# Optimization experiments

Hardware: AMD Instinct MI355X
Metric: run time of the kernel (lower is better)

Reference implementation:

```python
import jax, jax.numpy as jnp
import numpy as np


def setup_inputs() -> dict:
    key = jax.random.key(0)
    k1, k2, k3 = jax.random.split(key, 3)
    B, T, C = 4, 2048, 1024
    dim = C
    x = jax.random.normal(k1, (B, T, C), dtype=jnp.float32)
    # torch nn.Linear weight layout: [out_features, in_features], scaled like kaiming-uniform-ish
    w_qkv = jax.random.normal(k2, (3 * dim, dim), dtype=jnp.float32) * (1.0 / np.sqrt(dim))
    w_out = jax.random.normal(k3, (dim, dim), dtype=jnp.float32) * (1.0 / np.sqrt(dim))
    return {"x": x, "w_qkv": w_qkv, "w_out": w_out}


def reference(x, w_qkv, w_out):
    B, T, C = x.shape
    n_heads = 16
    head_dim = C // n_heads

    qkv = jnp.einsum("btc,dc->btd", x, w_qkv)  # [B,T,3C]
    q, k, v = jnp.split(qkv, 3, axis=-1)

    def split_heads(t):
        return t.reshape(B, T, n_heads, head_dim).transpose(0, 2, 1, 3)  # [B,H,T,hd]

    q, k, v = split_heads(q), split_heads(k), split_heads(v)

    scale = 1.0 / np.sqrt(head_dim).astype(np.float32)
    scores = jnp.einsum("bhqd,bhkd->bhqk", q, k) * scale  # [B,H,T,T]
    causal = jnp.tril(jnp.ones((T, T), dtype=bool))
    scores = jnp.where(causal, scores, jnp.finfo(scores.dtype).min)
    attn = jax.nn.softmax(scores, axis=-1)
    out = jnp.einsum("bhqk,bhkd->bhqd", attn, v)  # [B,H,T,hd]
    out = out.transpose(0, 2, 1, 3).reshape(B, T, C)
    return jnp.einsum("btc,dc->btd", out, w_out)
```

## Files before the change

kernel.cpp:

```cpp
#include <hip/hip_runtime.h>
#include <hip/hip_bf16.h>


typedef __attribute__((ext_vector_type(8))) short bf16x8;
typedef __attribute__((ext_vector_type(4))) float f32x4;
typedef __attribute__((ext_vector_type(16))) float f32x16;
typedef __attribute__((ext_vector_type(2))) unsigned uint2v;

#define GLOBAL_AS __attribute__((address_space(1)))
#define LDS_AS __attribute__((address_space(3)))

__device__ __forceinline__ unsigned short f2b_rne(float f) {
  unsigned u = __float_as_uint(f);
  unsigned r = u + 0x7fffu + ((u >> 16) & 1u);
  return (unsigned short)(r >> 16);
}

__device__ __forceinline__ unsigned cvt_pk_bf16(float lo, float hi) {
  unsigned r;
  asm("v_cvt_pk_bf16_f32 %0, %1, %2" : "=v"(r) : "v"(lo), "v"(hi));
  return r;
}

__device__ __forceinline__ void gload_lds16(const void* g, void* l) {
  __builtin_amdgcn_global_load_lds((const GLOBAL_AS void*)g, (LDS_AS void*)l, 16, 0, 0);
}

__global__ void f32_to_bf16_vec(const float* __restrict__ src,
                                unsigned short* __restrict__ dst, int n4) {
  int i = blockIdx.x * blockDim.x + threadIdx.x;
  int stride = gridDim.x * blockDim.x;
  for (; i < n4; i += stride) {
    float4 v = reinterpret_cast<const float4*>(src)[i];
    ushort4 o;
    o.x = f2b_rne(v.x); o.y = f2b_rne(v.y);
    o.z = f2b_rne(v.z); o.w = f2b_rne(v.w);
    reinterpret_cast<ushort4*>(dst)[i] = o;
  }
}

__global__ __launch_bounds__(256)
void v_transpose(const unsigned short* __restrict__ qkv,
                 unsigned short* __restrict__ vt) {
  __shared__ __align__(16) unsigned short Ts[64][64];
  const int tc = blockIdx.x, bh = blockIdx.y;
  const int b = bh >> 4, hed = bh & 15;
  const int t0 = tc * 64;
  const int tid = threadIdx.x;
  {
    const int r = tid >> 2, cb = (tid & 3) * 2;
    const unsigned short* src =
        qkv + (size_t)(b * 2048 + t0 + r) * 3072 + 2048 + hed * 64;
    bf16x8 v0 = *(const bf16x8*)(src + cb * 8);
    bf16x8 v1 = *(const bf16x8*)(src + cb * 8 + 8);
    *(bf16x8*)&Ts[r][(cb ^ (r & 7)) * 8] = v0;
    *(bf16x8*)&Ts[r][((cb + 1) ^ (r & 7)) * 8] = v1;
  }
  __syncthreads();
  const int d = tid >> 2;
  unsigned short* dst = vt + ((size_t)bh * 64 + d) * 2048 + t0;
#pragma unroll
  for (int tb2 = 0; tb2 < 2; ++tb2) {
    int tb = (tid & 3) * 2 + tb2;
    union { unsigned short s[8]; bf16x8 v; } o;
#pragma unroll
    for (int i = 0; i < 8; ++i) {
      int row = tb * 8 + i;
      o.s[i] = Ts[row][(((d >> 3) ^ (row & 7)) * 8) + (d & 7)];
    }
    *(bf16x8*)(dst + tb * 8) = o.v;
  }
}

template <int OUT_BF16>
__global__ __launch_bounds__(256)
void gemm_nt(const unsigned short* __restrict__ A,
             const unsigned short* __restrict__ B,
             void* __restrict__ Cout, int M, int N, int K) {
  __shared__ __align__(16) unsigned short As[128][32];
  __shared__ __align__(16) unsigned short Bs[128][32];
  const int tid = threadIdx.x;
  const int w = tid >> 6, lane = tid & 63;
  const int l16 = lane & 15, lg = lane >> 4;
  const int wrow = (w >> 1) * 64, wcol = (w & 1) * 64;
  const int m0 = blockIdx.y * 128, n0 = blockIdx.x * 128;

  f32x4 acc[4][4] = {};

  auto stage = [&](int k0) {
#pragma unroll
    for (int c2 = 0; c2 < 2; ++c2) {
      int c = 2 * w + c2;
      const unsigned short* ga =
          A + (size_t)(m0 + 16 * c + (lane >> 2)) * K + k0 + (lane & 3) * 8;
      gload_lds16(ga, &As[16 * c][0]);
      const unsigned short* gb =
          B + (size_t)(n0 + 16 * c + (lane >> 2)) * K + k0 + (lane & 3) * 8;
      gload_lds16(gb, &Bs[16 * c][0]);
    }
  };

  stage(0);
  __syncthreads();
  const int nk = K >> 5;
  for (int ks = 0; ks < nk; ++ks) {
    bf16x8 af[4], bfr[4];
#pragma unroll
    for (int mi = 0; mi < 4; ++mi)
      af[mi] = *(const bf16x8*)&As[wrow + mi * 16 + l16][lg * 8];
#pragma unroll
    for (int ni = 0; ni < 4; ++ni)
      bfr[ni] = *(const bf16x8*)&Bs[wcol + ni * 16 + l16][lg * 8];
    __syncthreads();
    if (ks + 1 < nk) stage((ks + 1) * 32);
#pragma unroll
    for (int mi = 0; mi < 4; ++mi)
#pragma unroll
      for (int ni = 0; ni < 4; ++ni)
        acc[mi][ni] = __builtin_amdgcn_mfma_f32_16x16x32_bf16(
            af[mi], bfr[ni], acc[mi][ni], 0, 0, 0);
    __syncthreads();
  }

#pragma unroll
  for (int mi = 0; mi < 4; ++mi) {
#pragma unroll
    for (int ni = 0; ni < 4; ++ni) {
#pragma unroll
      for (int j = 0; j < 4; ++j) {
        int row = m0 + wrow + mi * 16 + lg * 4 + j;
        int col = n0 + wcol + ni * 16 + l16;
        if (OUT_BF16) {
          ((unsigned short*)Cout)[(size_t)row * N + col] =
              f2b_rne(acc[mi][ni][j]);
        } else {
          ((float*)Cout)[(size_t)row * N + col] = acc[mi][ni][j];
        }
      }
    }
  }
}

__global__ __launch_bounds__(256)
void attn_fwd(const unsigned short* __restrict__ qkv,
              const unsigned short* __restrict__ vt,
              unsigned short* __restrict__ out) {
  const int T = 2048, C3 = 3072;
  __shared__ __align__(16) unsigned short Ks[2][64][64];
  __shared__ __align__(16) unsigned short Vs[2][64][64];
  __shared__ float Bc[4][32];

  const int tid = threadIdx.x, w = tid >> 6, lane = tid & 63;
  const int l31 = lane & 31, h = lane >> 5;
  const int wgid = (blockIdx.x & 7) * 128 + (blockIdx.x >> 3);
  const int qt = 15 - (wgid & 15);
  const int bh = wgid >> 4;
  const int b = bh >> 4, hed = bh & 15;
  const int qw = qt * 128 + w * 32;
  const size_t rowbase = (size_t)b * T * C3;
  const int hoff = hed * 64;
  const unsigned short* vbase = vt + (size_t)bh * 64 * 2048;
  const float c2 = 0.18033688f;

  auto stageK = [&](int kv0, int buf) {
#pragma unroll
    for (int pp = 0; pp < 2; ++pp) {
      int chunk = w * 2 + pp;
      int row = chunk * 8 + (lane >> 3);
      int blk = (lane & 7) ^ (lane >> 3);
      gload_lds16(
          qkv + rowbase + (size_t)(kv0 + row) * C3 + 1024 + hoff + blk * 8,
          &Ks[buf][chunk * 8][0]);
    }
  };
  auto stageV = [&](int kv0, int buf) {
#pragma unroll
    for (int pp = 0; pp < 2; ++pp) {
      int chunk = w * 2 + pp;
      int drow = chunk * 8 + (lane >> 3);
      int blk = (lane & 7) ^ (lane >> 3);
      gload_lds16(vbase + (size_t)drow * 2048 + kv0 + blk * 8,
                  &Vs[buf][chunk * 8][0]);
    }
  };

  bf16x8 qf[4];
  {
    const unsigned short* qp =
        qkv + rowbase + (size_t)(qw + l31) * C3 + hoff + h * 8;
#pragma unroll
    for (int s = 0; s < 4; ++s) qf[s] = *(const bf16x8*)(qp + 16 * s);
  }

  f32x16 oacc[2] = {};
  float m_r = -1e30f, sum = 0.f;

  stageK(0, 0);
  stageV(0, 0);

  int cur = 0;
  const int ntiles = qt * 2 + 2;
  for (int t = 0; t < ntiles; ++t) {
    const int kv0 = t * 64;
    __builtin_amdgcn_s_barrier();
    if (t + 1 < ntiles) {
      stageK(kv0 + 64, cur ^ 1);
      stageV(kv0 + 64, cur ^ 1);
      asm volatile("s_waitcnt vmcnt(4)" ::: "memory");
    } else {
      asm volatile("s_waitcnt vmcnt(0)" ::: "memory");
    }
    __builtin_amdgcn_s_barrier();
    __builtin_amdgcn_sched_barrier(0);

    if (kv0 <= qw) {
      f32x16 sacc[2] = {};
      __builtin_amdgcn_s_setprio(1);
#pragma unroll
      for (int s = 0; s < 4; ++s) {
#pragma unroll
        for (int kt = 0; kt < 2; ++kt) {
          int row = kt * 32 + l31;
          int blk = (2 * s + h) ^ (row & 7);
          bf16x8 kf = *(const bf16x8*)&Ks[cur][row][blk * 8];
          sacc[kt] = __builtin_amdgcn_mfma_f32_32x32x16_bf16(kf, qf[s],
                                                             sacc[kt], 0, 0, 0);
        }
      }
      __builtin_amdgcn_s_setprio(0);
      if (kv0 + 64 > qw) {
        int q_abs = qw + l31;
#pragma unroll
        for (int kt = 0; kt < 2; ++kt)
#pragma unroll
          for (int r = 0; r < 16; ++r) {
            int kv_abs = kv0 + kt * 32 + (r & 3) + 8 * (r >> 2) + 4 * h;
            if (kv_abs > q_abs) sacc[kt][r] = -1e30f;
          }
      }
      float mx[8];
#pragma unroll
      for (int g = 0; g < 8; ++g)
        mx[g] = fmaxf(fmaxf(sacc[g >> 2][(g & 3) * 4 + 0],
                            sacc[g >> 2][(g & 3) * 4 + 1]),
                      fmaxf(sacc[g >> 2][(g & 3) * 4 + 2],
                            sacc[g >> 2][(g & 3) * 4 + 3]));
      float tm = fmaxf(fmaxf(fmaxf(mx[0], mx[1]), fmaxf(mx[2], mx[3])),
                       fmaxf(fmaxf(mx[4], mx[5]), fmaxf(mx[6], mx[7])));
      tm = fmaxf(tm, __shfl_xor(tm, 32));
      if (t == 0) {
        m_r = tm;
      } else if (!__all(tm <= m_r + 16.0f)) {
        float mnew = fmaxf(m_r, tm);
        float corr = __builtin_amdgcn_exp2f((m_r - mnew) * c2);
        sum *= corr;
        if (h == 0) Bc[w][l31] = corr;
        m_r = mnew;
        asm volatile("s_waitcnt lgkmcnt(0)" ::: "memory");
#pragma unroll
        for (int r = 0; r < 16; ++r) {
          float cr = Bc[w][(r & 3) + 8 * (r >> 2) + 4 * h];
          oacc[0][r] *= cr;
          oacc[1][r] *= cr;
        }
      }
      float m2 = m_r * c2;
      float s0 = 0.f, s1 = 0.f, s2 = 0.f, s3 = 0.f;
#pragma unroll
      for (int kt = 0; kt < 2; ++kt)
#pragma unroll
        for (int r = 0; r < 16; r += 4) {
          float p0 = __builtin_amdgcn_exp2f(fmaf(sacc[kt][r + 0], c2, -m2));
          float p1 = __builtin_amdgcn_exp2f(fmaf(sacc[kt][r + 1], c2, -m2));
          float p2 = __builtin_amdgcn_exp2f(fmaf(sacc[kt][r + 2], c2, -m2));
          float p3 = __builtin_amdgcn_exp2f(fmaf(sacc[kt][r + 3], c2, -m2));
          sacc[kt][r + 0] = p0; sacc[kt][r + 1] = p1;
          sacc[kt][r + 2] = p2; sacc[kt][r + 3] = p3;
          s0 += p0; s1 += p1; s2 += p2; s3 += p3;
        }
      float sl = (s0 + s1) + (s2 + s3);
      sum += sl + __shfl_xor(sl, 32);
      unsigned pk[16];
#pragma unroll
      for (int kt = 0; kt < 2; ++kt)
#pragma unroll
        for (int r = 0; r < 16; r += 2)
          pk[kt * 8 + (r >> 1)] = cvt_pk_bf16(sacc[kt][r], sacc[kt][r + 1]);
      __builtin_amdgcn_s_setprio(1);
#pragma unroll
      for (int sg = 0; sg < 4; ++sg) {
        const int kt = sg >> 1, s = sg & 1;
        const int base = kt * 8 + 4 * s;
        uint2v r02 = __builtin_amdgcn_permlane32_swap(pk[base], pk[base + 2],
                                                      false, false);
        uint2v r13 = __builtin_amdgcn_permlane32_swap(pk[base + 1], pk[base + 3],
                                                      false, false);
        union { unsigned u[4]; bf16x8 v; } A;
        A.u[0] = r02.x; A.u[1] = r13.x;
        A.u[2] = r02.y; A.u[3] = r13.y;
#pragma unroll
        for (int dt = 0; dt < 2; ++dt) {
          int d = dt * 32 + l31;
          int blk = (2 * sg + h) ^ (d & 7);
          bf16x8 vf = *(const bf16x8*)&Vs[cur][d][blk * 8];
          oacc[dt] = __builtin_amdgcn_mfma_f32_32x32x16_bf16(A.v, vf,
                                                             oacc[dt], 0, 0, 0);
        }
      }
      __builtin_amdgcn_s_setprio(0);
    }
    cur ^= 1;
  }

  if (h == 0) Bc[w][l31] = 1.0f / sum;
  asm volatile("s_waitcnt lgkmcnt(0)" ::: "memory");
#pragma unroll
  for (int r = 0; r < 16; ++r) {
    int ql = (r & 3) + 8 * (r >> 2) + 4 * h;
    float inv = Bc[w][ql];
    int q_abs = qw + ql;
#pragma unroll
    for (int dt = 0; dt < 2; ++dt) {
      out[(size_t)(b * T + q_abs) * 1024 + hoff + dt * 32 + l31] =
          f2b_rne(oacc[dt][r] * inv);
    }
  }
}

extern "C" void kernel_launch(void* const* d_in, const int* in_sizes, int n_in,
                              void* d_out, int out_size, void* d_ws,
                              size_t ws_size, hipStream_t stream) {
  const float* x = (const float*)d_in[0];
  const float* w_qkv = (const float*)d_in[1];
  const float* w_out = (const float*)d_in[2];
  float* out = (float*)d_out;

  const int M = 8192, C = 1024, C3 = 3072;

  unsigned short* xb = (unsigned short*)d_ws;
  unsigned short* wqkvb = xb + (size_t)M * C;
  unsigned short* woutb = wqkvb + (size_t)C3 * C;
  unsigned short* qkv = woutb + (size_t)C * C;
  unsigned short* vtb = qkv + (size_t)M * C3;
  unsigned short* attno = xb;

  f32_to_bf16_vec<<<1024, 256, 0, stream>>>(x, xb, M * C / 4);
  f32_to_bf16_vec<<<512, 256, 0, stream>>>(w_qkv, wqkvb, C3 * C / 4);
  f32_to_bf16_vec<<<256, 256, 0, stream>>>(w_out, woutb, C * C / 4);

  gemm_nt<1><<<dim3(C3 / 128, M / 128), 256, 0, stream>>>(xb, wqkvb, qkv,
                                                          M, C3, C);

  v_transpose<<<dim3(32, 64), 256, 0, stream>>>(qkv, vtb);

  attn_fwd<<<1024, 256, 0, stream>>>(qkv, vtb, attno);

  gemm_nt<0><<<dim3(C / 128, M / 128), 256, 0, stream>>>(attno, woutb, out,
                                                         M, C, C);
}
```

Measured before the change: 211.1 us.

## Add dedicated QKV GEMM with 256x128 tiles, 32x32 MFMA and double buffering

Replaces the generic 128x128 bf16-output GEMM used for the QKV projection with a specialized kernel. It uses 512 threads, 256x128 output tiles, K-step 64, XOR-swizzled LDS, double-buffered async global-to-LDS loads and 32x32x16 MFMAs, plus an XCD-aware block remap. The aim is more reuse per LDS load, fewer barriers, and overlap of loads with compute in the largest GEMM. The cost is more LDS per block (about 96KB), which limits occupancy, and hardcoded shapes.

```diff
diff --git a/kernel.cpp b/kernel.cpp
--- a/kernel.cpp
+++ b/kernel.cpp
@@ -72,11 +72,106 @@
   }
 }
 
-template <int OUT_BF16>
+__global__ __launch_bounds__(512, 2)
+void gemm_qkv(const unsigned short* __restrict__ A,
+              const unsigned short* __restrict__ B,
+              unsigned short* __restrict__ C) {
+  const int K = 1024, N = 3072;
+  __shared__ __align__(16) unsigned short As[2][2][128 * 64];
+  __shared__ __align__(16) unsigned short Bs[2][128 * 64];
+
+  const int tid = threadIdx.x, wid = tid >> 6, lane = tid & 63;
+  const int l31 = lane & 31, h = lane >> 5;
+  const int wgid = ((int)blockIdx.x & 7) * 96 + ((int)blockIdx.x >> 3);
+  const int bx = wgid % 24, by = wgid / 24;
+  const int m0 = by * 256, n0 = bx * 128;
+  const int wr = wid >> 1, wc = wid & 1;
+
+  auto stage = [&](int t, int buf) {
+    const int k0 = t * 64;
+    const int r8 = lane >> 3;
+    const int blk = (lane & 7) ^ r8;
+#pragma unroll
+    for (int hh = 0; hh < 2; ++hh)
+#pragma unroll
+      for (int r = 0; r < 2; ++r) {
+        int row = r * 64 + wid * 8 + r8;
+        gload_lds16(A + (size_t)(m0 + hh * 128 + row) * K + k0 + blk * 8,
+                    &As[buf][hh][r * 4096 + wid * 512]);
+      }
+#pragma unroll
+    for (int r = 0; r < 2; ++r) {
+      int row = r * 64 + wid * 8 + r8;
+      gload_lds16(B + (size_t)(n0 + row) * K + k0 + blk * 8,
+                  &Bs[buf][r * 4096 + wid * 512]);
+    }
+  };
+
+  f32x16 acc[2][2] = {};
+
+  stage(0, 0);
+  asm volatile("s_waitcnt vmcnt(0)" ::: "memory");
+  __builtin_amdgcn_sched_barrier(0);
+  __builtin_amdgcn_s_barrier();
+  __builtin_amdgcn_sched_barrier(0);
+
+  int cur = 0;
+  for (int t = 0; t < 16; ++t) {
+    if (t + 1 < 16) stage(t + 1, cur ^ 1);
+
+    bf16x8 af[2][4], bfr[2][4];
+#pragma unroll
+    for (int mi = 0; mi < 2; ++mi) {
+      int row = (wr & 1) * 64 + mi * 32 + l31;
+#pragma unroll
+      for (int ks = 0; ks < 4; ++ks) {
+        int chunk = (ks * 2 + h) ^ (row & 7);
+        af[mi][ks] = *(const bf16x8*)&As[cur][wr >> 1][row * 64 + chunk * 8];
+      }
+    }
+#pragma unroll
+    for (int ni = 0; ni < 2; ++ni) {
+      int row = wc * 64 + ni * 32 + l31;
+#pragma unroll
+      for (int ks = 0; ks < 4; ++ks) {
+        int chunk = (ks * 2 + h) ^ (row & 7);
+        bfr[ni][ks] = *(const bf16x8*)&Bs[cur][row * 64 + chunk * 8];
+      }
+    }
+    __builtin_amdgcn_s_setprio(1);
+#pragma unroll
+    for (int ks = 0; ks < 4; ++ks)
+#pragma unroll
+      for (int mi = 0; mi < 2; ++mi)
+#pragma unroll
+        for (int ni = 0; ni < 2; ++ni)
+          acc[mi][ni] = __builtin_amdgcn_mfma_f32_32x32x16_bf16(
+              af[mi][ks], bfr[ni][ks], acc[mi][ni], 0, 0, 0);
+    __builtin_amdgcn_s_setprio(0);
+
+    asm volatile("s_waitcnt vmcnt(0)" ::: "memory");
+    __builtin_amdgcn_sched_barrier(0);
+    __builtin_amdgcn_s_barrier();
+    __builtin_amdgcn_sched_barrier(0);
+    cur ^= 1;
+  }
+
+#pragma unroll
+  for (int mi = 0; mi < 2; ++mi)
+#pragma unroll
+    for (int ni = 0; ni < 2; ++ni)
+#pragma unroll
+      for (int reg = 0; reg < 16; ++reg) {
+        int row = m0 + wr * 64 + mi * 32 + (reg & 3) + 8 * (reg >> 2) + 4 * h;
+        int col = n0 + wc * 64 + ni * 32 + l31;
+        C[(size_t)row * N + col] = f2b_rne(acc[mi][ni][reg]);
+      }
+}
+
 __global__ __launch_bounds__(256)
 void gemm_nt(const unsigned short* __restrict__ A,
              const unsigned short* __restrict__ B,
-             void* __restrict__ Cout, int M, int N, int K) {
+             float* __restrict__ Cout, int M, int N, int K) {
   __shared__ __align__(16) unsigned short As[128][32];
   __shared__ __align__(16) unsigned short Bs[128][32];
   const int tid = threadIdx.x;
@@ -123,22 +218,15 @@
   }
 
 #pragma unroll
-  for (int mi = 0; mi < 4; ++mi) {
-#pragma unroll
-    for (int ni = 0; ni < 4; ++ni) {
+  for (int mi = 0; mi < 4; ++mi)
+#pragma unroll
+    for (int ni = 0; ni < 4; ++ni)
 #pragma unroll
       for (int j = 0; j < 4; ++j) {
         int row = m0 + wrow + mi * 16 + lg * 4 + j;
         int col = n0 + wcol + ni * 16 + l16;
-        if (OUT_BF16) {
-          ((unsigned short*)Cout)[(size_t)row * N + col] =
-              f2b_rne(acc[mi][ni][j]);
-        } else {
-          ((float*)Cout)[(size_t)row * N + col] = acc[mi][ni][j];
-        }
-      }
-    }
-  }
+        Cout[(size_t)row * N + col] = acc[mi][ni][j];
+      }
 }
 
 __global__ __launch_bounds__(256)
@@ -295,15 +383,15 @@
                                                       false, false);
         uint2v r13 = __builtin_amdgcn_permlane32_swap(pk[base + 1], pk[base + 3],
                                                       false, false);
-        union { unsigned u[4]; bf16x8 v; } A;
-        A.u[0] = r02.x; A.u[1] = r13.x;
-        A.u[2] = r02.y; A.u[3] = r13.y;
+        union { unsigned u[4]; bf16x8 v; } Afr;
+        Afr.u[0] = r02.x; Afr.u[1] = r13.x;
+        Afr.u[2] = r02.y; Afr.u[3] = r13.y;
 #pragma unroll
         for (int dt = 0; dt < 2; ++dt) {
           int d = dt * 32 + l31;
           int blk = (2 * sg + h) ^ (d & 7);
           bf16x8 vf = *(const bf16x8*)&Vs[cur][d][blk * 8];
-          oacc[dt] = __builtin_amdgcn_mfma_f32_32x32x16_bf16(A.v, vf,
+          oacc[dt] = __builtin_amdgcn_mfma_f32_32x32x16_bf16(Afr.v, vf,
                                                              oacc[dt], 0, 0, 0);
         }
       }
@@ -348,13 +436,12 @@
   f32_to_bf16_vec<<<512, 256, 0, stream>>>(w_qkv, wqkvb, C3 * C / 4);
   f32_to_bf16_vec<<<256, 256, 0, stream>>>(w_out, woutb, C * C / 4);
 
-  gemm_nt<1><<<dim3(C3 / 128, M / 128), 256, 0, stream>>>(xb, wqkvb, qkv,
-                                                          M, C3, C);
+  gemm_qkv<<<768, 512, 0, stream>>>(xb, wqkvb, qkv);
 
   v_transpose<<<dim3(32, 64), 256, 0, stream>>>(qkv, vtb);
 
   attn_fwd<<<1024, 256, 0, stream>>>(qkv, vtb, attno);
 
-  gemm_nt<0><<<dim3(C / 128, M / 128), 256, 0, stream>>>(attno, woutb, out,
-                                                         M, C, C);
-}
+  gemm_nt<<<dim3(C / 128, M / 128), 256, 0, stream>>>(attno, woutb, out,
+                                                      M, C, C);
+}
```

New measurement: 203.5 us. 1.04x faster.
